# Kernel optimization log

Hardware: AMD Instinct MI355X
Metric: run time of the kernel (lower is better)

Reference implementation:

```python
import jax, jax.numpy as jnp
import numpy as np

B, C, V = 1024, 512, 256  # batch, num_conjunctions, num_variables


def setup_inputs() -> dict:
    key = jax.random.key(0)
    k1, k2, k3 = jax.random.split(key, 3)
    x0 = jax.random.uniform(k1, (B, V), dtype=jnp.float32)
    # torch init: conj = 1 - 2*rand  -> uniform in (-1, 1)
    conjunctions = 1.0 - 2.0 * jax.random.uniform(k2, (C, 2 * V), dtype=jnp.float32)
    # rw = 10 - 20*rand -> uniform in (-10, 10)
    rule_weights = 10.0 - 20.0 * jax.random.uniform(k3, (C,), dtype=jnp.float32)
    return {"x0": x0, "conjunctions": conjunctions, "rule_weights": rule_weights}


def reference(x0, conjunctions, rule_weights):
    mu = jax.nn.sigmoid(conjunctions)            # (C, 2V)
    x = jnp.concatenate((x0, 1.0 - x0), axis=1)  # (B, 2V)
    # fuzzy-AND: broadcast mul-add then min over literal axis
    x_pot = mu[None, :, :] * x[:, None, :] + (1.0 - mu)[None, :, :]  # (B, C, 2V)
    fit = jnp.min(x_pot, axis=-1)                # (B, C)
    return 5.0 + jnp.sum(rule_weights * fit, axis=-1)  # (B,)
```

## Files before the change

### kernel.cpp

```cpp
#include <hip/hip_runtime.h>


#define B_    1024
#define C_    512
#define V_    256
#define TWOV  512

#define BPB    8
#define NBG    (B_ / BPB)
#define NCH    4

typedef float f32x4 __attribute__((ext_vector_type(4)));

__global__ __launch_bounds__(256) void k_prep(const float* __restrict__ conj,
                                              float2* __restrict__ muT2,
                                              float* __restrict__ out) {
    const int c = blockIdx.x;
    const int v = threadIdx.x;
    if (c < 4) out[c * 256 + v] = 5.0f;
    float z1 = conj[(size_t)c * TWOV + v];
    float z2 = conj[(size_t)c * TWOV + V_ + v];
    float m1 = 1.0f / (1.0f + __expf(-z1));
    float m2 = 1.0f / (1.0f + __expf(-z2));
    muT2[(size_t)(v >> 1) * (2 * C_) + c * 2 + (v & 1)] = make_float2(m1, m2);
}

__global__ __launch_bounds__(512, 4) void k_main(const float* __restrict__ x0,
                                                 const f32x4* __restrict__ muT4,
                                                 const float* __restrict__ rw,
                                                 float* __restrict__ out) {
    const int tid  = threadIdx.x;
    const int lane = tid & 63;
    const int wave = tid >> 6;
    const int t    = wave & 1;
    const int s    = wave >> 1;
    const int bg   = blockIdx.x;
    const int chunk= blockIdx.y;
    const int c    = chunk * 128 + t * 64 + lane;
    const int xq   = s * 16;

    __shared__ f32x4 xs4[BPB * V_ / 4];
    __shared__ float red[4 * 128 * 9];

    {
        const f32x4* xg = reinterpret_cast<const f32x4*>(x0 + (size_t)bg * BPB * V_);
        xs4[tid] = xg[tid];
    }

    const f32x4* mu1p = muT4 + (size_t)(s * 32) * C_ + c;
    const f32x4* mu2p = mu1p + C_;

    float m[BPB];
#pragma unroll
    for (int i = 0; i < BPB; ++i) m[i] = 0.0f;

    f32x4 A0, B0, A1, B1, A2, B2;

#define MULOAD(DST, PTR) \
    asm volatile("global_load_dwordx4 %0, %1, off" : "=v"(DST) : "v"(PTR))
#define ISSUE(MA, MB) do { \
    MULOAD(MA, mu1p); MULOAD(MB, mu2p); \
    mu1p += 2 * C_; mu2p += 2 * C_; } while (0)

    ISSUE(A0, B0);
    ISSUE(A1, B1);

    __syncthreads();

#define COMPUTE(q, MA, MB) do { \
    _Pragma("unroll") \
    for (int bi = 0; bi < BPB; ++bi) { \
        f32x4 xc = xs4[bi * 64 + xq + (q)]; \
        float mm = m[bi]; \
        mm = fmaxf(fmaxf(__builtin_fmaf(-MA.x, xc.x, MA.x), MA.y * xc.x), mm); \
        mm = fmaxf(fmaxf(__builtin_fmaf(-MA.z, xc.y, MA.z), MA.w * xc.y), mm); \
        mm = fmaxf(fmaxf(__builtin_fmaf(-MB.x, xc.z, MB.x), MB.y * xc.z), mm); \
        mm = fmaxf(fmaxf(__builtin_fmaf(-MB.z, xc.w, MB.z), MB.w * xc.w), mm); \
        m[bi] = mm; \
    } } while (0)

#define QSTEP(q, MAC, MBC, MAN, MBN) do { \
    ISSUE(MAN, MBN); \
    asm volatile("s_waitcnt vmcnt(4)" : "+v"(MAC), "+v"(MBC)); \
    COMPUTE(q, MAC, MBC); } while (0)

    QSTEP( 0, A0, B0, A2, B2);
    QSTEP( 1, A1, B1, A0, B0);
    QSTEP( 2, A2, B2, A1, B1);
    QSTEP( 3, A0, B0, A2, B2);
    QSTEP( 4, A1, B1, A0, B0);
    QSTEP( 5, A2, B2, A1, B1);
    QSTEP( 6, A0, B0, A2, B2);
    QSTEP( 7, A1, B1, A0, B0);
    QSTEP( 8, A2, B2, A1, B1);
    QSTEP( 9, A0, B0, A2, B2);
    QSTEP(10, A1, B1, A0, B0);
    QSTEP(11, A2, B2, A1, B1);
    QSTEP(12, A0, B0, A2, B2);
    QSTEP(13, A1, B1, A0, B0);
    asm volatile("s_waitcnt vmcnt(2)" : "+v"(A2), "+v"(B2));
    COMPUTE(14, A2, B2);
    asm volatile("s_waitcnt vmcnt(0)" : "+v"(A0), "+v"(B0));
    COMPUTE(15, A0, B0);

#undef QSTEP
#undef COMPUTE
#undef ISSUE
#undef MULOAD

    const int ci = t * 64 + lane;
#pragma unroll
    for (int bi = 0; bi < BPB; ++bi)
        red[(s * 128 + ci) * 9 + bi] = m[bi];
    __syncthreads();

    if (wave < 2) {
        const float rwc = rw[c];
        float con0, con1, con2, con3, con4, con5, con6, con7;
#define FIN(bi, CON) do { \
        float mm = red[(0 * 128 + ci) * 9 + bi]; \
        mm = fmaxf(mm, red[(1 * 128 + ci) * 9 + bi]); \
        mm = fmaxf(mm, red[(2 * 128 + ci) * 9 + bi]); \
        mm = fmaxf(mm, red[(3 * 128 + ci) * 9 + bi]); \
        float v = rwc * (1.0f - mm); \
        v += __shfl_xor(v, 1, 64);  v += __shfl_xor(v, 2, 64); \
        v += __shfl_xor(v, 4, 64);  v += __shfl_xor(v, 8, 64); \
        v += __shfl_xor(v, 16, 64); v += __shfl_xor(v, 32, 64); \
        CON = v; } while (0)
        FIN(0, con0); FIN(1, con1); FIN(2, con2); FIN(3, con3);
        FIN(4, con4); FIN(5, con5); FIN(6, con6); FIN(7, con7);
#undef FIN
        float t0 = (lane & 1) ? con1 : con0;
        float t1 = (lane & 1) ? con3 : con2;
        float t2 = (lane & 1) ? con5 : con4;
        float t3 = (lane & 1) ? con7 : con6;
        float u0 = (lane & 2) ? t1 : t0;
        float u1 = (lane & 2) ? t3 : t2;
        float sel = (lane & 4) ? u1 : u0;
        if (lane < 8)
            atomicAdd(&out[bg * BPB + lane], sel);
    }
}

__global__ __launch_bounds__(256) void k_naive(const float* __restrict__ x0,
                                               const float* __restrict__ conj,
                                               const float* __restrict__ rw,
                                               float* __restrict__ out) {
    int b = blockIdx.x;
    int t = threadIdx.x;
    __shared__ float red[256];
    float acc = 0.0f;
    for (int c = t; c < C_; c += 256) {
        float mm = 0.0f;
        for (int v = 0; v < V_; ++v) {
            float mu1 = 1.0f / (1.0f + expf(-conj[(size_t)c * TWOV + v]));
            float mu2 = 1.0f / (1.0f + expf(-conj[(size_t)c * TWOV + V_ + v]));
            float x = x0[(size_t)b * V_ + v];
            mm = fmaxf(mm, fmaxf(mu1 * (1.0f - x), mu2 * x));
        }
        acc += rw[c] * (1.0f - mm);
    }
    red[t] = acc;
    __syncthreads();
    for (int s = 128; s > 0; s >>= 1) {
        if (t < s) red[t] += red[t + s];
        __syncthreads();
    }
    if (t == 0) out[b] = 5.0f + red[0];
}

extern "C" void kernel_launch(void* const* d_in, const int* in_sizes, int n_in,
                              void* d_out, int out_size, void* d_ws, size_t ws_size,
                              hipStream_t stream) {
    const float* x0   = (const float*)d_in[0];
    const float* conj = (const float*)d_in[1];
    const float* rw   = (const float*)d_in[2];
    float* out = (float*)d_out;

    const size_t mu_floats = (size_t)(V_ / 2) * C_ * 4;
    const size_t need = mu_floats * sizeof(float);

    if (ws_size < need) {
        k_naive<<<B_, 256, 0, stream>>>(x0, conj, rw, out);
        return;
    }

    f32x4* muT4 = (f32x4*)d_ws;

    k_prep<<<C_, 256, 0, stream>>>(conj, (float2*)muT4, out);
    dim3 grid(NBG, NCH);
    k_main<<<grid, 512, 0, stream>>>(x0, muT4, rw, out);
}
```

Before: 22.67 us.

## Split literal axis across all eight waves, each covering two conjunctions

```diff
diff --git a/kernel.cpp b/kernel.cpp
--- a/kernel.cpp
+++ b/kernel.cpp
@@ -32,96 +32,91 @@
     const int tid  = threadIdx.x;
     const int lane = tid & 63;
     const int wave = tid >> 6;
-    const int t    = wave & 1;
-    const int s    = wave >> 1;
     const int bg   = blockIdx.x;
     const int chunk= blockIdx.y;
-    const int c    = chunk * 128 + t * 64 + lane;
-    const int xq   = s * 16;
+    const int cA   = chunk * 128 + lane;
+    const int vq   = wave * 8;
 
     __shared__ f32x4 xs4[BPB * V_ / 4];
-    __shared__ float red[4 * 128 * 9];
+    __shared__ float red[8 * 64 * 17];
 
     {
         const f32x4* xg = reinterpret_cast<const f32x4*>(x0 + (size_t)bg * BPB * V_);
         xs4[tid] = xg[tid];
     }
 
-    const f32x4* mu1p = muT4 + (size_t)(s * 32) * C_ + c;
-    const f32x4* mu2p = mu1p + C_;
+    const f32x4* pA  = muT4 + (size_t)(wave * 16) * C_ + cA;
+    const f32x4* pA1 = pA + C_;
 
-    float m[BPB];
+    float mA[BPB], mB[BPB];
 #pragma unroll
-    for (int i = 0; i < BPB; ++i) m[i] = 0.0f;
+    for (int i = 0; i < BPB; ++i) { mA[i] = 0.0f; mB[i] = 0.0f; }
 
-    f32x4 A0, B0, A1, B1, A2, B2;
+    f32x4 A0a, A1a, B0a, B1a, A0b, A1b, B0b, B1b, A0c, A1c, B0c, B1c;
 
-#define MULOAD(DST, PTR) \
-    asm volatile("global_load_dwordx4 %0, %1, off" : "=v"(DST) : "v"(PTR))
-#define ISSUE(MA, MB) do { \
-    MULOAD(MA, mu1p); MULOAD(MB, mu2p); \
-    mu1p += 2 * C_; mu2p += 2 * C_; } while (0)
+#define ISSUE(A0, A1, Bq0, Bq1) do { \
+    asm volatile("global_load_dwordx4 %0, %1, off"             : "=v"(A0)  : "v"(pA));  \
+    asm volatile("global_load_dwordx4 %0, %1, off offset:1024" : "=v"(Bq0) : "v"(pA));  \
+    asm volatile("global_load_dwordx4 %0, %1, off"             : "=v"(A1)  : "v"(pA1)); \
+    asm volatile("global_load_dwordx4 %0, %1, off offset:1024" : "=v"(Bq1) : "v"(pA1)); \
+    pA += 2 * C_; pA1 += 2 * C_; } while (0)
 
-    ISSUE(A0, B0);
-    ISSUE(A1, B1);
+    ISSUE(A0a, A1a, B0a, B1a);
+    ISSUE(A0b, A1b, B0b, B1b);
 
     __syncthreads();
 
-#define COMPUTE(q, MA, MB) do { \
+#define COMPUTE(q, A0, A1, Bq0, Bq1) do { \
     _Pragma("unroll") \
     for (int bi = 0; bi < BPB; ++bi) { \
-        f32x4 xc = xs4[bi * 64 + xq + (q)]; \
-        float mm = m[bi]; \
-        mm = fmaxf(fmaxf(__builtin_fmaf(-MA.x, xc.x, MA.x), MA.y * xc.x), mm); \
-        mm = fmaxf(fmaxf(__builtin_fmaf(-MA.z, xc.y, MA.z), MA.w * xc.y), mm); \
-        mm = fmaxf(fmaxf(__builtin_fmaf(-MB.x, xc.z, MB.x), MB.y * xc.z), mm); \
-        mm = fmaxf(fmaxf(__builtin_fmaf(-MB.z, xc.w, MB.z), MB.w * xc.w), mm); \
-        m[bi] = mm; \
+        f32x4 xc = xs4[bi * 64 + vq + (q)]; \
+        float ma = mA[bi], mb = mB[bi]; \
+        ma = fmaxf(fmaxf(__builtin_fmaf(-A0.x,  xc.x, A0.x),  A0.y  * xc.x), ma); \
+        ma = fmaxf(fmaxf(__builtin_fmaf(-A0.z,  xc.y, A0.z),  A0.w  * xc.y), ma); \
+        ma = fmaxf(fmaxf(__builtin_fmaf(-A1.x,  xc.z, A1.x),  A1.y  * xc.z), ma); \
+        ma = fmaxf(fmaxf(__builtin_fmaf(-A1.z,  xc.w, A1.z),  A1.w  * xc.w), ma); \
+        mb = fmaxf(fmaxf(__builtin_fmaf(-Bq0.x, xc.x, Bq0.x), Bq0.y * xc.x), mb); \
+        mb = fmaxf(fmaxf(__builtin_fmaf(-Bq0.z, xc.y, Bq0.z), Bq0.w * xc.y), mb); \
+        mb = fmaxf(fmaxf(__builtin_fmaf(-Bq1.x, xc.z, Bq1.x), Bq1.y * xc.z), mb); \
+        mb = fmaxf(fmaxf(__builtin_fmaf(-Bq1.z, xc.w, Bq1.z), Bq1.w * xc.w), mb); \
+        mA[bi] = ma; mB[bi] = mb; \
     } } while (0)
 
-#define QSTEP(q, MAC, MBC, MAN, MBN) do { \
-    ISSUE(MAN, MBN); \
-    asm volatile("s_waitcnt vmcnt(4)" : "+v"(MAC), "+v"(MBC)); \
-    COMPUTE(q, MAC, MBC); } while (0)
+#define QSTEP(q, CA0, CA1, CB0, CB1, NA0, NA1, NB0, NB1) do { \
+    ISSUE(NA0, NA1, NB0, NB1); \
+    asm volatile("s_waitcnt vmcnt(8)" : "+v"(CA0), "+v"(CA1), "+v"(CB0), "+v"(CB1)); \
+    COMPUTE(q, CA0, CA1, CB0, CB1); } while (0)
 
-    QSTEP( 0, A0, B0, A2, B2);
-    QSTEP( 1, A1, B1, A0, B0);
-    QSTEP( 2, A2, B2, A1, B1);
-    QSTEP( 3, A0, B0, A2, B2);
-    QSTEP( 4, A1, B1, A0, B0);
-    QSTEP( 5, A2, B2, A1, B1);
-    QSTEP( 6, A0, B0, A2, B2);
-    QSTEP( 7, A1, B1, A0, B0);
-    QSTEP( 8, A2, B2, A1, B1);
-    QSTEP( 9, A0, B0, A2, B2);
-    QSTEP(10, A1, B1, A0, B0);
-    QSTEP(11, A2, B2, A1, B1);
-    QSTEP(12, A0, B0, A2, B2);
-    QSTEP(13, A1, B1, A0, B0);
-    asm volatile("s_waitcnt vmcnt(2)" : "+v"(A2), "+v"(B2));
-    COMPUTE(14, A2, B2);
-    asm volatile("s_waitcnt vmcnt(0)" : "+v"(A0), "+v"(B0));
-    COMPUTE(15, A0, B0);
+    QSTEP(0, A0a, A1a, B0a, B1a,  A0c, A1c, B0c, B1c);
+    QSTEP(1, A0b, A1b, B0b, B1b,  A0a, A1a, B0a, B1a);
+    QSTEP(2, A0c, A1c, B0c, B1c,  A0b, A1b, B0b, B1b);
+    QSTEP(3, A0a, A1a, B0a, B1a,  A0c, A1c, B0c, B1c);
+    QSTEP(4, A0b, A1b, B0b, B1b,  A0a, A1a, B0a, B1a);
+    QSTEP(5, A0c, A1c, B0c, B1c,  A0b, A1b, B0b, B1b);
+    asm volatile("s_waitcnt vmcnt(4)" : "+v"(A0a), "+v"(A1a), "+v"(B0a), "+v"(B1a));
+    COMPUTE(6, A0a, A1a, B0a, B1a);
+    asm volatile("s_waitcnt vmcnt(0)" : "+v"(A0b), "+v"(A1b), "+v"(B0b), "+v"(B1b));
+    COMPUTE(7, A0b, A1b, B0b, B1b);
 
 #undef QSTEP
 #undef COMPUTE
 #undef ISSUE
-#undef MULOAD
 
-    const int ci = t * 64 + lane;
 #pragma unroll
-    for (int bi = 0; bi < BPB; ++bi)
-        red[(s * 128 + ci) * 9 + bi] = m[bi];
+    for (int bi = 0; bi < BPB; ++bi) {
+        red[(wave * 64 + lane) * 17 + bi * 2 + 0] = mA[bi];
+        red[(wave * 64 + lane) * 17 + bi * 2 + 1] = mB[bi];
+    }
     __syncthreads();
 
     if (wave < 2) {
-        const float rwc = rw[c];
+        const float rwc = rw[chunk * 128 + wave * 64 + lane];
         float con0, con1, con2, con3, con4, con5, con6, con7;
 #define FIN(bi, CON) do { \
-        float mm = red[(0 * 128 + ci) * 9 + bi]; \
-        mm = fmaxf(mm, red[(1 * 128 + ci) * 9 + bi]); \
-        mm = fmaxf(mm, red[(2 * 128 + ci) * 9 + bi]); \
-        mm = fmaxf(mm, red[(3 * 128 + ci) * 9 + bi]); \
+        float mm = red[(0 * 64 + lane) * 17 + (bi) * 2 + wave]; \
+        _Pragma("unroll") \
+        for (int wv = 1; wv < 8; ++wv) \
+            mm = fmaxf(mm, red[(wv * 64 + lane) * 17 + (bi) * 2 + wave]); \
         float v = rwc * (1.0f - mm); \
         v += __shfl_xor(v, 1, 64);  v += __shfl_xor(v, 2, 64); \
         v += __shfl_xor(v, 4, 64);  v += __shfl_xor(v, 8, 64); \
```

Measured after the change: 22.86 us. Within noise of the previous version (+0.9%).
